# Performance work log

Measured on AMD Instinct MI355X. Metric: run time of the kernel, lower is better.

The kernel has to match this reference:

```python
import jax, jax.numpy as jnp
import numpy as np

C = 128
B, H, W = 32, 64, 64


def _lstm(x, Wih, Whh, b, reverse):
    """Batched LSTM, PyTorch gate order (i, f, g, o).
    x: [N, T, C] -> h: [N, T, C]. reverse=True scans backward but returns
    outputs aligned to the original time axis (matches torch bidirectional)."""
    N = x.shape[0]
    Ch = Whh.shape[1]
    xp = jnp.einsum('ntc,gc->ntg', x, Wih) + b  # precomputed input projection [N,T,4C]

    def step(carry, xt):
        h, c = carry
        z = xt + h @ Whh.T
        i, f, g, o = jnp.split(z, 4, axis=-1)
        c = jax.nn.sigmoid(f) * c + jax.nn.sigmoid(i) * jnp.tanh(g)
        h = jax.nn.sigmoid(o) * jnp.tanh(c)
        return (h, c), h

    init = (jnp.zeros((N, Ch), x.dtype), jnp.zeros((N, Ch), x.dtype))
    _, hs = jax.lax.scan(step, init, jnp.swapaxes(xp, 0, 1), reverse=reverse)
    return jnp.swapaxes(hs, 0, 1)


def _conv1x1(x, w, b):
    # x: [B, C, s1, s2]; w: [O, C]; b: [O]
    return jnp.einsum('bcxy,oc->boxy', x, w) + b[None, :, None, None]


def setup_inputs() -> dict:
    key = jax.random.key(0)
    ks = jax.random.split(key, 24)
    k = 1.0 / np.sqrt(C)
    u = lambda kk, shp: jax.random.uniform(kk, shp, jnp.float32, -k, k)
    inp = {'x': jax.random.normal(ks[0], (B, C, H, W), jnp.float32)}
    names = ['vWih_f', 'vWhh_f', 'vb_f', 'vWih_b', 'vWhh_b', 'vb_b',
             'hWih_f', 'hWhh_f', 'hb_f', 'hWih_b', 'hWhh_b', 'hb_b']
    shapes = [(4 * C, C), (4 * C, C), (4 * C,)] * 4
    for i, (n, s) in enumerate(zip(names, shapes)):
        inp[n] = u(ks[1 + i], s)
    for i, n in enumerate(['down', 'up', 'right', 'left']):
        inp['w_' + n] = u(ks[13 + 2 * i], (C, C))
        inp['b_' + n] = u(ks[14 + 2 * i], (C,))
    return inp


def reference(x, vWih_f, vWhh_f, vb_f, vWih_b, vWhh_b, vb_b,
              hWih_f, hWhh_f, hb_f, hWih_b, hWhh_b, hb_b,
              w_down, b_down, w_up, b_up, w_right, b_right, w_left, b_left):
    Bn, Cn, Hn, Wn = x.shape
    xt = jnp.transpose(x, (0, 3, 2, 1))  # [B, W, H, C]  (torch transpose(1,3))

    # vertical LSTM: torch loops i over H, seq over W -> batch rows into B*H
    xv = jnp.transpose(xt, (0, 2, 1, 3)).reshape(Bn * Hn, Wn, Cn)  # [B*H, W, C]
    hv_f = _lstm(xv, vWih_f, vWhh_f, vb_f, False).reshape(Bn, Hn, Wn, Cn)
    hv_b = _lstm(xv, vWih_b, vWhh_b, vb_b, True).reshape(Bn, Hn, Wn, Cn)
    # stack over H at dim2 then transpose(1,3) -> [B, C, H, W]
    x_up = _conv1x1(jnp.transpose(hv_f, (0, 3, 1, 2)), w_up, b_up)
    x_down = _conv1x1(jnp.transpose(hv_b, (0, 3, 1, 2)), w_down, b_down)

    # horizontal LSTM: torch loops i over W, seq over H -> batch cols into B*W
    xh = xt.reshape(Bn * Wn, Hn, Cn)  # [B*W, H, C]
    hh_f = _lstm(xh, hWih_f, hWhh_f, hb_f, False).reshape(Bn, Wn, Hn, Cn)
    hh_b = _lstm(xh, hWih_b, hWhh_b, hb_b, True).reshape(Bn, Wn, Hn, Cn)
    # stack over W at dim2 gives [B, H, W, C]; transpose(1,3) -> [B, C, W, H]
    x_right = _conv1x1(jnp.transpose(hh_f, (0, 3, 1, 2)), w_right, b_right)
    x_left = _conv1x1(jnp.transpose(hh_b, (0, 3, 1, 2)), w_left, b_left)

    return (x_down, x_up, x_right, x_left)
```

## Files before the change

kernel.cpp:

```cpp
#include <hip/hip_runtime.h>
#include <stdint.h>

#define OUTSZ  (32*128*64*64)

typedef short bf16x8 __attribute__((ext_vector_type(8)));
typedef float f32x4  __attribute__((ext_vector_type(4)));

__device__ __forceinline__ uint16_t f2bf(float f) {
  union { float f; uint32_t u; } v; v.f = f;
  uint32_t u = v.u;
  u += 0x7fffu + ((u >> 16) & 1u);
  return (uint16_t)(u >> 16);
}

__device__ __forceinline__ float sigf(float x) {
  return __builtin_amdgcn_rcpf(1.f + __expf(-x));
}
__device__ __forceinline__ float tanh2s(float x) {
  float e = __expf(-2.f * x);
  return __builtin_amdgcn_rcpf(1.f + e) * 2.f - 1.f;
}

__global__ void transpose_x(const float* __restrict__ x, uint16_t* __restrict__ xn) {
  const int h = blockIdx.x, b = blockIdx.y;
  __shared__ float tile[128][65];
  const int tid = threadIdx.x;
  #pragma unroll
  for (int it = 0; it < 32; ++it) {
    int idx = it * 256 + tid;
    int c = idx >> 6, w = idx & 63;
    tile[c][w] = x[(((b * 128 + c) * 64 + h) << 6) + w];
  }
  __syncthreads();
  uint32_t* out = (uint32_t*)(xn + ((size_t)(b * 64 + h) * 64) * 128);
  #pragma unroll
  for (int it = 0; it < 16; ++it) {
    int idx = it * 256 + tid;
    int w = idx >> 6, cd = idx & 63;
    uint32_t lo = f2bf(tile[cd * 2][w]);
    uint32_t hi = f2bf(tile[cd * 2 + 1][w]);
    out[w * 64 + cd] = lo | (hi << 16);
  }
}

struct PrepArgs { const float* s[12]; };

__global__ void prep_weights(PrepArgs a, uint16_t* __restrict__ wbuf,
                             uint16_t* __restrict__ wcbuf) {
  int idx = blockIdx.x * 256 + threadIdx.x;
  if (idx < 524288) {
    int m = idx >> 16;
    wbuf[idx] = f2bf(a.s[m][idx & 65535]);
  } else {
    int j = idx - 524288;
    if (j < 65536) {
      int m = j >> 14;
      wcbuf[j] = f2bf(a.s[8 + m][j & 16383]);
    }
  }
}

__global__ __launch_bounds__(512, 2) void lstm_kernel(
    const uint16_t* __restrict__ xn,
    const uint16_t* __restrict__ wbuf,
    const float* __restrict__ bvf, const float* __restrict__ bvb,
    const float* __restrict__ bhf, const float* __restrict__ bhb,
    uint16_t* __restrict__ hbuf)
{
  const int dir  = blockIdx.y;
  const int seq0 = blockIdx.x * 32;
  const int tid  = threadIdx.x;
  const int wv   = tid >> 6;
  const int lane = tid & 63;
  const int l15  = lane & 15;
  const int l4   = lane >> 4;
  const int mycol = wv * 16 + l15;
  const bool rev   = (dir & 1);
  const bool horiz = (dir >= 2);

  const uint16_t* wih = wbuf + (size_t)(2 * dir) * (512 * 128);
  const uint16_t* whh = wih + 512 * 128;
  const float* bias = (dir == 0) ? bvf : (dir == 1) ? bvb : (dir == 2) ? bhf : bhb;
  uint16_t* hout = hbuf + (size_t)dir * ((size_t)2048 * 64 * 128);

  bf16x8 Bih[4][4], Bhh[4][4];
  {
    const int base = mycol * 128 + l4 * 8;
    #pragma unroll
    for (int g = 0; g < 4; ++g)
      #pragma unroll
      for (int kc = 0; kc < 4; ++kc) {
        Bih[g][kc] = *(const bf16x8*)(wih + base + g * (128 * 128) + kc * 32);
        Bhh[g][kc] = *(const bf16x8*)(whh + base + g * (128 * 128) + kc * 32);
      }
  }
  f32x4 biav[4];
  #pragma unroll
  for (int g = 0; g < 4; ++g) {
    float b = bias[mycol + 128 * g];
    f32x4 bs = {b, b, b, b};
    biav[g] = bs;
  }

  __shared__ __attribute__((aligned(16))) uint16_t ring[8][32][136];
  {
    uint32_t* p = (uint32_t*)&ring[7][0][0];
    for (int i = tid; i < 2176; i += 512) p[i] = 0;
  }
  __syncthreads();

  int xbase[2];
  #pragma unroll
  for (int mt = 0; mt < 2; ++mt) {
    int seq = seq0 + mt * 16 + l15;
    xbase[mt] = horiz ? (((seq >> 6) * 4096 + (seq & 63)) * 128)
                      : (seq * (64 * 128));
  }
  const int tstride = horiz ? (64 * 128) : 128;

  float cst[2][4];
  #pragma unroll
  for (int mt = 0; mt < 2; ++mt)
    #pragma unroll
    for (int r = 0; r < 4; ++r) cst[mt][r] = 0.f;

  const int drow   = tid >> 4;
  const int dchunk = tid & 15;
  const int dpc8   = dchunk ^ ((drow >> 2) & 3);

  auto dump_slot = [&](int g, int s) {
    bf16x8 v = *(const bf16x8*)(&ring[s][drow][dpc8 * 8]);
    int stepl = g * 8 + s;
    int t = rev ? 63 - stepl : stepl;
    *(bf16x8*)(hout + ((size_t)(seq0 + drow) * 64 + t) * 128 + dchunk * 8) = v;
  };

  const int swz = (l15 >> 2) & 3;

  f32x4 acc[2][4];

  auto gate_math = [&](int mt, int slot) {
    float h[4];
    #pragma unroll
    for (int r = 0; r < 4; ++r) {
      float zi = acc[mt][0][r];
      float zf = acc[mt][1][r];
      float zg = acc[mt][2][r];
      float zo = acc[mt][3][r];
      float c = sigf(zf) * cst[mt][r] + sigf(zi) * tanh2s(zg);
      cst[mt][r] = c;
      h[r] = sigf(zo) * tanh2s(c);
    }
    uint16_t* a0 = &ring[slot][mt * 16 + l4 * 4][((mycol >> 3) ^ l4) * 8 + (mycol & 7)];
    #pragma unroll
    for (int p = 0; p < 2; ++p) {
      uint32_t v;
      asm("v_cvt_pk_bf16_f32 %0, %1, %2" : "=v"(v) : "v"(h[2 * p]), "v"(h[2 * p + 1]));
      uint16_t* ap = a0 + (2 * p) * 136;
      ap[0]   = (uint16_t)v;
      ap[136] = (uint16_t)(v >> 16);
    }
  };

  auto ih_mt = [&](int mt, bf16x8 (&ax)[2][4]) {
    #pragma unroll
    for (int g = 0; g < 4; ++g)
      acc[mt][g] = __builtin_amdgcn_mfma_f32_16x16x32_bf16(ax[mt][0], Bih[g][0], biav[g], 0, 0, 0);
    #pragma unroll
    for (int kc = 1; kc < 4; ++kc)
      #pragma unroll
      for (int g = 0; g < 4; ++g)
        acc[mt][g] = __builtin_amdgcn_mfma_f32_16x16x32_bf16(ax[mt][kc], Bih[g][kc], acc[mt][g], 0, 0, 0);
  };

  auto do_step = [&](int step, bf16x8 (&axc)[2][4], bf16x8 (&axn)[2][4]) {
    (void)axc;
    const int tn_l = (step < 63) ? step + 1 : 63;
    const int tn   = rev ? 63 - tn_l : tn_l;
    #pragma unroll
    for (int mt = 0; mt < 2; ++mt)
      #pragma unroll
      for (int kc = 0; kc < 4; ++kc)
        axn[mt][kc] = *(const bf16x8*)(xn + xbase[mt] + tn * tstride + kc * 32 + l4 * 8);

    const int prev = (step + 7) & 7;
    const int slot = step & 7;

    #pragma unroll
    for (int kc = 0; kc < 4; ++kc) {
      bf16x8 ah = *(const bf16x8*)(&ring[prev][l15][((kc * 4 + l4) ^ swz) * 8]);
      #pragma unroll
      for (int g = 0; g < 4; ++g)
        acc[0][g] = __builtin_amdgcn_mfma_f32_16x16x32_bf16(ah, Bhh[g][kc], acc[0][g], 0, 0, 0);
    }
    #pragma unroll
    for (int kc = 0; kc < 4; ++kc) {
      bf16x8 ah = *(const bf16x8*)(&ring[prev][16 + l15][((kc * 4 + l4) ^ swz) * 8]);
      #pragma unroll
      for (int g = 0; g < 4; ++g)
        acc[1][g] = __builtin_amdgcn_mfma_f32_16x16x32_bf16(ah, Bhh[g][kc], acc[1][g], 0, 0, 0);
    }
    gate_math(0, slot);

    if (step >= 7) dump_slot(((step + 1) >> 3) - 1, (step + 1) & 7);

    if (step < 63) ih_mt(0, axn);
    gate_math(1, slot);
    if (step < 63) ih_mt(1, axn);

    asm volatile("s_waitcnt lgkmcnt(0)" ::: "memory");
    __builtin_amdgcn_s_barrier();
    __builtin_amdgcn_sched_barrier(0);
  };

  bf16x8 axA[2][4], axB[2][4];
  {
    const int t0 = rev ? 63 : 0;
    #pragma unroll
    for (int mt = 0; mt < 2; ++mt)
      #pragma unroll
      for (int kc = 0; kc < 4; ++kc)
        axA[mt][kc] = *(const bf16x8*)(xn + xbase[mt] + t0 * tstride + kc * 32 + l4 * 8);
  }
  ih_mt(0, axA);
  ih_mt(1, axA);
  for (int s2 = 0; s2 < 64; s2 += 2) {
    do_step(s2,     axA, axB);
    do_step(s2 + 1, axB, axA);
  }
  #pragma unroll
  for (int s = 1; s < 8; ++s) dump_slot(7, s);
}

__global__ __launch_bounds__(256, 2) void conv_kernel(
    const uint16_t* __restrict__ hbuf, const uint16_t* __restrict__ wc,
    const float* __restrict__ b_down, const float* __restrict__ b_up,
    const float* __restrict__ b_right, const float* __restrict__ b_left,
    float* __restrict__ out)
{
  const int d   = blockIdx.y;
  const int P0  = blockIdx.x * 128;
  const int tid = threadIdx.x;
  const int wv = tid >> 6, lane = tid & 63, l15 = lane & 15, l4 = lane >> 4;

  const int lstm_dir = (d == 0) ? 1 : (d == 1) ? 0 : d;
  const uint16_t* hb = hbuf + (size_t)lstm_dir * ((size_t)2048 * 64 * 128);
  const uint16_t* w  = wc + d * (128 * 128);
  const float* bias = (d == 0) ? b_down : (d == 1) ? b_up : (d == 2) ? b_right : b_left;
  float* outp = out + (size_t)d * OUTSZ;

  bf16x8 Bf[2][4];
  float bc[2];
  #pragma unroll
  for (int j = 0; j < 2; ++j) {
    int o = (2 * wv + j) * 16 + l15;
    bc[j] = bias[o];
    #pragma unroll
    for (int kc = 0; kc < 4; ++kc)
      Bf[j][kc] = *(const bf16x8*)(w + o * 128 + kc * 32 + l4 * 8);
  }

  const f32x4 vzero = {0.f, 0.f, 0.f, 0.f};
  f32x4 acc[8][2];
  #pragma unroll
  for (int mt = 0; mt < 8; ++mt) { acc[mt][0] = vzero; acc[mt][1] = vzero; }

  #pragma unroll
  for (int kc = 0; kc < 4; ++kc) {
    bf16x8 A[8];
    #pragma unroll
    for (int mt = 0; mt < 8; ++mt) {
      int p = P0 + mt * 16 + l15;
      A[mt] = *(const bf16x8*)(hb + (size_t)p * 128 + kc * 32 + l4 * 8);
    }
    #pragma unroll
    for (int mt = 0; mt < 8; ++mt)
      #pragma unroll
      for (int j = 0; j < 2; ++j)
        acc[mt][j] = __builtin_amdgcn_mfma_f32_16x16x32_bf16(A[mt], Bf[j][kc], acc[mt][j], 0, 0, 0);
  }

  __shared__ __attribute__((aligned(16))) float olds[64][132];
  const int bb = P0 >> 12, s0 = P0 & 4095;
  float* obase = outp + ((size_t)bb * 128) * 4096 + s0;

  #pragma unroll
  for (int j = 0; j < 2; ++j) {
    if (j) __syncthreads();
    #pragma unroll
    for (int mt = 0; mt < 8; ++mt) {
      f32x4 v = acc[mt][j] + bc[j];
      *(f32x4*)(&olds[wv * 16 + l15][(mt * 4 + l4) * 4]) = v;
    }
    __syncthreads();
    #pragma unroll
    for (int it = 0; it < 8; ++it) {
      int flat = (it * 256 + tid) * 4;
      int ol = flat >> 7, s = flat & 127;
      int o = (ol >> 4) * 32 + j * 16 + (ol & 15);
      f32x4 v = *(const f32x4*)(&olds[ol][s]);
      *(f32x4*)(obase + (size_t)o * 4096 + s) = v;
    }
  }
}

extern "C" void kernel_launch(void* const* d_in, const int* in_sizes, int n_in,
                              void* d_out, int out_size, void* d_ws, size_t ws_size,
                              hipStream_t stream) {
  const float* x = (const float*)d_in[0];
  uint16_t* ws    = (uint16_t*)d_ws;
  uint16_t* xn    = ws;
  uint16_t* wbuf  = xn + 16777216;
  uint16_t* wcbuf = wbuf + 524288;
  uint16_t* hbuf  = wcbuf + 65536;

  transpose_x<<<dim3(64, 32), 256, 0, stream>>>(x, xn);

  PrepArgs pa;
  const int widx[12] = {1, 2, 4, 5, 7, 8, 10, 11, 13, 15, 17, 19};
  for (int i = 0; i < 12; ++i) pa.s[i] = (const float*)d_in[widx[i]];
  prep_weights<<<2304, 256, 0, stream>>>(pa, wbuf, wcbuf);

  lstm_kernel<<<dim3(64, 4), 512, 0, stream>>>(
      xn, wbuf,
      (const float*)d_in[3], (const float*)d_in[6],
      (const float*)d_in[9], (const float*)d_in[12],
      hbuf);

  conv_kernel<<<dim3(1024, 4), 256, 0, stream>>>(
      hbuf, wcbuf,
      (const float*)d_in[14], (const float*)d_in[16],
      (const float*)d_in[18], (const float*)d_in[20],
      (float*)d_out);
}
```

Baseline: 587.4 us.

## Fold exp2 scaling into weights, fuse gate reciprocals, and interleave MFMA with gate math

```diff
diff --git a/kernel.cpp b/kernel.cpp
--- a/kernel.cpp
+++ b/kernel.cpp
@@ -5,20 +5,14 @@
 
 typedef short bf16x8 __attribute__((ext_vector_type(8)));
 typedef float f32x4  __attribute__((ext_vector_type(4)));
+
+#define SGB(mask, n) __builtin_amdgcn_sched_group_barrier((mask), (n), 0)
 
 __device__ __forceinline__ uint16_t f2bf(float f) {
   union { float f; uint32_t u; } v; v.f = f;
   uint32_t u = v.u;
   u += 0x7fffu + ((u >> 16) & 1u);
   return (uint16_t)(u >> 16);
-}
-
-__device__ __forceinline__ float sigf(float x) {
-  return __builtin_amdgcn_rcpf(1.f + __expf(-x));
-}
-__device__ __forceinline__ float tanh2s(float x) {
-  float e = __expf(-2.f * x);
-  return __builtin_amdgcn_rcpf(1.f + e) * 2.f - 1.f;
 }
 
 __global__ void transpose_x(const float* __restrict__ x, uint16_t* __restrict__ xn) {
@@ -50,7 +44,9 @@
   int idx = blockIdx.x * 256 + threadIdx.x;
   if (idx < 524288) {
     int m = idx >> 16;
-    wbuf[idx] = f2bf(a.s[m][idx & 65535]);
+    int row = (idx & 65535) >> 7;
+    float s = ((row >> 7) == 2) ? -2.88539008f : -1.44269504f;
+    wbuf[idx] = f2bf(s * a.s[m][idx & 65535]);
   } else {
     int j = idx - 524288;
     if (j < 65536) {
@@ -97,7 +93,8 @@
   f32x4 biav[4];
   #pragma unroll
   for (int g = 0; g < 4; ++g) {
-    float b = bias[mycol + 128 * g];
+    float s = (g == 2) ? -2.88539008f : -1.44269504f;
+    float b = s * bias[mycol + 128 * g];
     f32x4 bs = {b, b, b, b};
     biav[g] = bs;
   }
@@ -143,13 +140,18 @@
     float h[4];
     #pragma unroll
     for (int r = 0; r < 4; ++r) {
-      float zi = acc[mt][0][r];
-      float zf = acc[mt][1][r];
-      float zg = acc[mt][2][r];
-      float zo = acc[mt][3][r];
-      float c = sigf(zf) * cst[mt][r] + sigf(zi) * tanh2s(zg);
+      float e1 = __builtin_amdgcn_exp2f(acc[mt][0][r]);
+      float ef = __builtin_amdgcn_exp2f(acc[mt][1][r]);
+      float e2 = __builtin_amdgcn_exp2f(fminf(acc[mt][2][r], 126.f));
+      float eo = __builtin_amdgcn_exp2f(acc[mt][3][r]);
+      float rp = __builtin_amdgcn_rcpf((1.f + e1) * (1.f + e2));
+      float a  = (1.f - e2) * rp;
+      float sf = __builtin_amdgcn_rcpf(1.f + ef);
+      float c  = __builtin_fmaf(sf, cst[mt][r], a);
       cst[mt][r] = c;
-      h[r] = sigf(zo) * tanh2s(c);
+      float ec = __builtin_amdgcn_exp2f(fminf(c * -2.88539008f, 126.f));
+      float rq = __builtin_amdgcn_rcpf((1.f + eo) * (1.f + ec));
+      h[r] = (1.f - ec) * rq;
     }
     uint16_t* a0 = &ring[slot][mt * 16 + l4 * 4][((mycol >> 3) ^ l4) * 8 + (mycol & 7)];
     #pragma unroll
@@ -183,30 +185,56 @@
       for (int kc = 0; kc < 4; ++kc)
         axn[mt][kc] = *(const bf16x8*)(xn + xbase[mt] + tn * tstride + kc * 32 + l4 * 8);
 
+    {
+      int gd = ((step + 1) >> 3) - 1;
+      gd = (gd < 0) ? 0 : gd;
+      dump_slot(gd, (step + 1) & 7);
+    }
+
     const int prev = (step + 7) & 7;
     const int slot = step & 7;
 
+    bf16x8 ah0[4], ah1[4];
     #pragma unroll
     for (int kc = 0; kc < 4; ++kc) {
-      bf16x8 ah = *(const bf16x8*)(&ring[prev][l15][((kc * 4 + l4) ^ swz) * 8]);
+      ah0[kc] = *(const bf16x8*)(&ring[prev][l15][((kc * 4 + l4) ^ swz) * 8]);
+      ah1[kc] = *(const bf16x8*)(&ring[prev][16 + l15][((kc * 4 + l4) ^ swz) * 8]);
+    }
+
+    #pragma unroll
+    for (int kc = 0; kc < 4; ++kc)
       #pragma unroll
       for (int g = 0; g < 4; ++g)
-        acc[0][g] = __builtin_amdgcn_mfma_f32_16x16x32_bf16(ah, Bhh[g][kc], acc[0][g], 0, 0, 0);
-    }
-    #pragma unroll
-    for (int kc = 0; kc < 4; ++kc) {
-      bf16x8 ah = *(const bf16x8*)(&ring[prev][16 + l15][((kc * 4 + l4) ^ swz) * 8]);
+        acc[0][g] = __builtin_amdgcn_mfma_f32_16x16x32_bf16(ah0[kc], Bhh[g][kc], acc[0][g], 0, 0, 0);
+    #pragma unroll
+    for (int kc = 0; kc < 4; ++kc)
       #pragma unroll
       for (int g = 0; g < 4; ++g)
-        acc[1][g] = __builtin_amdgcn_mfma_f32_16x16x32_bf16(ah, Bhh[g][kc], acc[1][g], 0, 0, 0);
-    }
+        acc[1][g] = __builtin_amdgcn_mfma_f32_16x16x32_bf16(ah1[kc], Bhh[g][kc], acc[1][g], 0, 0, 0);
     gate_math(0, slot);
 
-    if (step >= 7) dump_slot(((step + 1) >> 3) - 1, (step + 1) & 7);
-
-    if (step < 63) ih_mt(0, axn);
+    SGB(0x100, 9);
+    SGB(0x020, 8);
+    #pragma unroll
+    for (int i = 0; i < 32; ++i) {
+      SGB(0x008, 1);
+      SGB(0x002, 3);
+      if ((i & 7) == 7) SGB(0x200, 1);
+    }
+    SGB(0x040, 1);
+    __builtin_amdgcn_sched_barrier(0);
+
+    ih_mt(0, axn);
     gate_math(1, slot);
-    if (step < 63) ih_mt(1, axn);
+    ih_mt(1, axn);
+
+    #pragma unroll
+    for (int i = 0; i < 32; ++i) {
+      SGB(0x008, 1);
+      SGB(0x002, 3);
+      if ((i & 7) == 7) SGB(0x200, 1);
+    }
+    __builtin_amdgcn_sched_barrier(0);
 
     asm volatile("s_waitcnt lgkmcnt(0)" ::: "memory");
     __builtin_amdgcn_s_barrier();
```

Result: slower. 703.2 us (+19.7%).
